# Kernel optimization log

Hardware: AMD Instinct MI355X
Metric: run time of the kernel (lower is better)

## Reference

```python
import jax, jax.numpy as jnp
import numpy as np

B, E, N1, K, CIN, CB, COUT, G = 2, 2048, 96, 32, 64, 32, 64, 4
NEG_SLOPE = 0.01  # nn.LeakyReLU default


def setup_inputs() -> dict:
    key = jax.random.key(0)
    ks = jax.random.split(key, 9)
    sites1 = jax.random.normal(ks[0], (B, N1, CIN), jnp.float32)
    sites2 = jax.random.normal(ks[1], (B, K, CIN), jnp.float32)
    bonds = jax.random.normal(ks[2], (B, E, CB), jnp.float32)
    idx1 = jax.random.randint(ks[3], (E,), 0, N1, jnp.int32)
    idx2 = jax.random.randint(ks[4], (E,), 0, K, jnp.int32)
    idx2_oh = jax.nn.one_hot(idx2, K, dtype=jnp.float32)  # [E, K]
    F = 2 * CIN + CB
    W_eq = jax.random.normal(ks[5], (G, F, COUT), jnp.float32) / np.float32(np.sqrt(F))
    b_eq = jnp.zeros((COUT,), jnp.float32)
    W_att = jax.random.normal(ks[6], (COUT, 1), jnp.float32) / np.float32(np.sqrt(COUT))
    b_att = jnp.zeros((1,), jnp.float32)
    # permutation group action on the K cells: identity + random perms
    perms = [jnp.arange(K, dtype=jnp.int32)]
    pk = ks[7]
    for _ in range(G - 1):
        pk, sk = jax.random.split(pk)
        perms.append(jax.random.permutation(sk, K).astype(jnp.int32))
    perms1 = jnp.stack(perms)  # [G, K]
    perms2 = perms1            # same action on input and output cell axes
    return dict(sites1=sites1, sites2=sites2, bonds=bonds, W_eq=W_eq, b_eq=b_eq,
                W_att=W_att, b_att=b_att, idx2_oh=idx2_oh, idx1=idx1, idx2=idx2,
                perms1=perms1, perms2=perms2)


def reference(sites1, sites2, bonds, W_eq, b_eq, W_att, b_att, idx2_oh, idx1, idx2, perms1, perms2):
    Bn = sites1.shape[0]
    Gn, Kn = perms1.shape
    On = W_eq.shape[2]
    # gather sender / receiver site features along the site axis
    sites_s = jnp.take(sites1, idx1, axis=1)              # [B,E,CIN]
    sites_r = jnp.take(sites2, idx2, axis=1)              # [B,E,CIN]
    vectors = jnp.concatenate([sites_s, sites_r, bonds], axis=2)  # [B,E,F]
    # outer-product expansion onto cells (idx2_oh is one-hot over K)
    vc = jnp.einsum('bef,ek->befk', vectors, idx2_oh)     # [B,E,F,K]
    # permutation-equivariant linear (group-averaged): per-group-element weight,
    # input cells permuted by perms1, output cells un-permuted by perms2
    xg = vc[:, :, :, perms1]                               # [B,E,F,G,K]
    yg = jnp.einsum('befgk,gfo->beogk', xg, W_eq)          # [B,E,O,G,K]
    inv2 = jnp.argsort(perms2, axis=1)                     # inverse perms [G,K]
    garr = jnp.arange(Gn)[:, None]
    y = yg[:, :, :, garr, inv2].mean(axis=3)               # [B,E,O,K]
    y = jax.nn.leaky_relu(y + b_eq[None, None, :, None], NEG_SLOPE)
    # gather each edge's receiving cell slot == dot with one-hot
    lat = jnp.einsum('beok,ek->beo', y, idx2_oh)           # [B,E,O]
    att = jax.nn.sigmoid(jnp.einsum('beo,oj->bej', lat, W_att) + b_att)  # [B,E,1]
    lat = att * lat
    # scatter_add over edges into receiving sites
    out = jnp.zeros((Bn, Kn, On), lat.dtype).at[:, idx2].add(lat)  # [B,K,O]
    return out
```

## Files before the change

kernel.cpp:

```cpp
#include <hip/hip_runtime.h>
#include <math.h>

#define Bn   2
#define En   2048
#define N1n  96
#define Kn   32
#define CINn 64
#define CBn  32
#define On   64
#define Gn   4
#define Fn   160
#define NEG  0.01f
#define NW   8
#define NT   (NW * 64)

__global__ void __launch_bounds__(NT, 1)
fused_kernel(const float* __restrict__ sites1, const float* __restrict__ sites2,
             const float* __restrict__ bonds,  const float* __restrict__ W_eq,
             const float* __restrict__ b_eq,   const float* __restrict__ W_att,
             const float* __restrict__ b_att,  const int* __restrict__ idx1,
             const int* __restrict__ idx2,     const int* __restrict__ perms1,
             const int* __restrict__ perms2,   float* __restrict__ out) {
    __shared__ float Weff[Fn][On];
    __shared__ float vbuf[NW][Fn];
    __shared__ float red[NW][On];
    __shared__ float s2[CINn];
    __shared__ float wgs[Gn];
    __shared__ int   elist[En];
    __shared__ int   ecount;

    const int t  = threadIdx.x;
    const int bk = blockIdx.x;
    const int b  = bk >> 5;
    const int k2 = bk & (Kn - 1);

    if (t < Gn) {
        int g = t, j = 0;
        for (; j < Kn; ++j) if (perms2[g * Kn + j] == k2) break;
        wgs[g] = (j < Kn && perms1[g * Kn + j] == k2) ? 1.f : 0.f;
    }
    if (t == Gn) ecount = 0;
    __syncthreads();

    {
        const float w0 = wgs[0], w1 = wgs[1], w2 = wgs[2], w3 = wgs[3];
        const float4* W4 = (const float4*)W_eq;
        float4* Wd = (float4*)&Weff[0][0];
        const int n4 = Fn * On / 4;
        for (int i = t; i < n4; i += NT) {
            float4 a0 = W4[i], a1 = W4[n4 + i], a2 = W4[2 * n4 + i], a3 = W4[3 * n4 + i];
            float4 r;
            r.x = 0.25f * (w0 * a0.x + w1 * a1.x + w2 * a2.x + w3 * a3.x);
            r.y = 0.25f * (w0 * a0.y + w1 * a1.y + w2 * a2.y + w3 * a3.y);
            r.z = 0.25f * (w0 * a0.z + w1 * a1.z + w2 * a2.z + w3 * a3.z);
            r.w = 0.25f * (w0 * a0.w + w1 * a1.w + w2 * a2.w + w3 * a3.w);
            Wd[i] = r;
        }
    }

    for (int e = t; e < En; e += NT)
        if (idx2[e] == k2) { int p = atomicAdd(&ecount, 1); elist[p] = e; }

    if (t < CINn) s2[t] = sites2[(b * Kn + k2) * CINn + t];
    __syncthreads();

    const int w    = t >> 6;
    const int lane = t & 63;
    const int og   = lane & 15;
    const int fg   = lane >> 4;

    const float4 be4 = ((const float4*)b_eq)[og];
    const float4 wa  = ((const float4*)W_att)[og];
    const float  ba  = b_att[0];
    const int    ec  = ecount;

    float4 oacc = make_float4(0.f, 0.f, 0.f, 0.f);

    for (int i = w; i < ec; i += NW) {
        const int e  = elist[i];
        const int i1 = idx1[e];

        vbuf[w][lane]        = sites1[(b * N1n + i1) * CINn + lane];
        vbuf[w][CINn + lane] = s2[lane];
        if (lane < CBn) vbuf[w][2 * CINn + lane] = bonds[(b * En + e) * CBn + lane];
        __builtin_amdgcn_wave_barrier();

        float4 acc = make_float4(0.f, 0.f, 0.f, 0.f);
#pragma unroll
        for (int fi = 0; fi < Fn / 4; ++fi) {
            const int f = 4 * fi + fg;
            const float  vf = vbuf[w][f];
            const float4 wv = *(const float4*)&Weff[f][og * 4];
            acc.x += vf * wv.x; acc.y += vf * wv.y;
            acc.z += vf * wv.z; acc.w += vf * wv.w;
        }
        __builtin_amdgcn_wave_barrier();

#pragma unroll
        for (int m = 16; m <= 32; m <<= 1) {
            acc.x += __shfl_xor(acc.x, m);
            acc.y += __shfl_xor(acc.y, m);
            acc.z += __shfl_xor(acc.z, m);
            acc.w += __shfl_xor(acc.w, m);
        }

        float4 lat;
        lat.x = acc.x + be4.x; lat.x = lat.x > 0.f ? lat.x : NEG * lat.x;
        lat.y = acc.y + be4.y; lat.y = lat.y > 0.f ? lat.y : NEG * lat.y;
        lat.z = acc.z + be4.z; lat.z = lat.z > 0.f ? lat.z : NEG * lat.z;
        lat.w = acc.w + be4.w; lat.w = lat.w > 0.f ? lat.w : NEG * lat.w;

        float part = lat.x * wa.x + lat.y * wa.y + lat.z * wa.z + lat.w * wa.w;
#pragma unroll
        for (int m = 1; m <= 8; m <<= 1) part += __shfl_xor(part, m);

        const float att = 1.f / (1.f + expf(-(part + ba)));
        oacc.x += att * lat.x;
        oacc.y += att * lat.y;
        oacc.z += att * lat.z;
        oacc.w += att * lat.w;
    }

    if (fg == 0) *(float4*)&red[w][og * 4] = oacc;
    __syncthreads();

    if (t < On) {
        float s = 0.f;
#pragma unroll
        for (int q = 0; q < NW; ++q) s += red[q][t];
        out[((size_t)b * Kn + k2) * On + t] = s;
    }
}

extern "C" void kernel_launch(void* const* d_in, const int* in_sizes, int n_in,
                              void* d_out, int out_size, void* d_ws, size_t ws_size,
                              hipStream_t stream) {
    const float* sites1 = (const float*)d_in[0];
    const float* sites2 = (const float*)d_in[1];
    const float* bonds  = (const float*)d_in[2];
    const float* W_eq   = (const float*)d_in[3];
    const float* b_eq   = (const float*)d_in[4];
    const float* W_att  = (const float*)d_in[5];
    const float* b_att  = (const float*)d_in[6];
    const int*   idx1   = (const int*)d_in[8];
    const int*   idx2   = (const int*)d_in[9];
    const int*   perms1 = (const int*)d_in[10];
    const int*   perms2 = (const int*)d_in[11];
    float* out = (float*)d_out;

    fused_kernel<<<Bn * Kn, NT, 0, stream>>>(
        sites1, sites2, bonds, W_eq, b_eq, W_att, b_att,
        idx1, idx2, perms1, perms2, out);
}
```

Measured before the change: 100.0 us.

## Batch eight edges per wave and hoist the constant receiver-site contribution

Each wave now loads eight edges' sender-site and bond features into shared memory at once. It then reuses every Weff float4 load across those eight accumulators, where before it ran one serial edge per iteration. The receiver-site part of the matvec is the same for every edge in a block, so it is computed once into p2 and used to seed the accumulators. This cuts redundant LDS traffic and serial loop latency and adds instruction-level parallelism. In exchange it uses more registers, and partial batches do duplicated padded work that is masked out.

```diff
diff --git a/kernel.cpp b/kernel.cpp
--- a/kernel.cpp
+++ b/kernel.cpp
@@ -13,6 +13,7 @@
 #define NEG  0.01f
 #define NW   8
 #define NT   (NW * 64)
+#define EB   8
 
 __global__ void __launch_bounds__(NT, 1)
 fused_kernel(const float* __restrict__ sites1, const float* __restrict__ sites2,
@@ -22,7 +23,7 @@
              const int* __restrict__ idx2,     const int* __restrict__ perms1,
              const int* __restrict__ perms2,   float* __restrict__ out) {
     __shared__ float Weff[Fn][On];
-    __shared__ float vbuf[NW][Fn];
+    __shared__ float vs[NW][EB][96];
     __shared__ float red[NW][On];
     __shared__ float s2[CINn];
     __shared__ float wgs[Gn];
@@ -68,57 +69,83 @@
     const int lane = t & 63;
     const int og   = lane & 15;
     const int fg   = lane >> 4;
+    const int ec   = ecount;
 
     const float4 be4 = ((const float4*)b_eq)[og];
     const float4 wa  = ((const float4*)W_att)[og];
     const float  ba  = b_att[0];
-    const int    ec  = ecount;
+
+    float4 p2 = make_float4(0.f, 0.f, 0.f, 0.f);
+#pragma unroll
+    for (int fi = 0; fi < 16; ++fi) {
+        const int f  = 64 + 4 * fi + fg;
+        const float  vf = s2[4 * fi + fg];
+        const float4 wv = *(const float4*)&Weff[f][og * 4];
+        p2.x += vf * wv.x; p2.y += vf * wv.y;
+        p2.z += vf * wv.z; p2.w += vf * wv.w;
+    }
 
     float4 oacc = make_float4(0.f, 0.f, 0.f, 0.f);
 
-    for (int i = w; i < ec; i += NW) {
-        const int e  = elist[i];
-        const int i1 = idx1[e];
+    for (int base = w * EB; base < ec; base += NW * EB) {
+        const int nb = (ec - base < EB) ? (ec - base) : EB;
 
-        vbuf[w][lane]        = sites1[(b * N1n + i1) * CINn + lane];
-        vbuf[w][CINn + lane] = s2[lane];
-        if (lane < CBn) vbuf[w][2 * CINn + lane] = bonds[(b * En + e) * CBn + lane];
+        __builtin_amdgcn_wave_barrier();
+#pragma unroll
+        for (int j = 0; j < EB; ++j) {
+            const int jj = j < nb ? j : nb - 1;
+            const int e  = elist[base + jj];
+            const int i1 = idx1[e];
+            vs[w][j][lane] = sites1[((b * N1n + i1) << 6) + lane];
+            if (lane < CBn) vs[w][j][CINn + lane] = bonds[(b * En + e) * CBn + lane];
+        }
         __builtin_amdgcn_wave_barrier();
 
-        float4 acc = make_float4(0.f, 0.f, 0.f, 0.f);
+        float4 acc[EB];
 #pragma unroll
-        for (int fi = 0; fi < Fn / 4; ++fi) {
-            const int f = 4 * fi + fg;
-            const float  vf = vbuf[w][f];
+        for (int j = 0; j < EB; ++j) acc[j] = p2;
+
+#pragma unroll
+        for (int fi = 0; fi < 24; ++fi) {
+            const int vsidx = 4 * fi + fg;
+            const int f     = vsidx < CINn ? vsidx : vsidx + CINn;
             const float4 wv = *(const float4*)&Weff[f][og * 4];
-            acc.x += vf * wv.x; acc.y += vf * wv.y;
-            acc.z += vf * wv.z; acc.w += vf * wv.w;
+#pragma unroll
+            for (int j = 0; j < EB; ++j) {
+                const float vf = vs[w][j][vsidx];
+                acc[j].x += vf * wv.x; acc[j].y += vf * wv.y;
+                acc[j].z += vf * wv.z; acc[j].w += vf * wv.w;
+            }
         }
         __builtin_amdgcn_wave_barrier();
 
 #pragma unroll
-        for (int m = 16; m <= 32; m <<= 1) {
-            acc.x += __shfl_xor(acc.x, m);
-            acc.y += __shfl_xor(acc.y, m);
-            acc.z += __shfl_xor(acc.z, m);
-            acc.w += __shfl_xor(acc.w, m);
+        for (int j = 0; j < EB; ++j) {
+            float4 a = acc[j];
+#pragma unroll
+            for (int m = 16; m <= 32; m <<= 1) {
+                a.x += __shfl_xor(a.x, m);
+                a.y += __shfl_xor(a.y, m);
+                a.z += __shfl_xor(a.z, m);
+                a.w += __shfl_xor(a.w, m);
+            }
+            float4 lat;
+            lat.x = a.x + be4.x; lat.x = lat.x > 0.f ? lat.x : NEG * lat.x;
+            lat.y = a.y + be4.y; lat.y = lat.y > 0.f ? lat.y : NEG * lat.y;
+            lat.z = a.z + be4.z; lat.z = lat.z > 0.f ? lat.z : NEG * lat.z;
+            lat.w = a.w + be4.w; lat.w = lat.w > 0.f ? lat.w : NEG * lat.w;
+
+            float part = lat.x * wa.x + lat.y * wa.y + lat.z * wa.z + lat.w * wa.w;
+#pragma unroll
+            for (int m = 1; m <= 8; m <<= 1) part += __shfl_xor(part, m);
+
+            float att = 1.f / (1.f + expf(-(part + ba)));
+            att *= (j < nb) ? 1.f : 0.f;
+            oacc.x += att * lat.x;
+            oacc.y += att * lat.y;
+            oacc.z += att * lat.z;
+            oacc.w += att * lat.w;
         }
-
-        float4 lat;
-        lat.x = acc.x + be4.x; lat.x = lat.x > 0.f ? lat.x : NEG * lat.x;
-        lat.y = acc.y + be4.y; lat.y = lat.y > 0.f ? lat.y : NEG * lat.y;
-        lat.z = acc.z + be4.z; lat.z = lat.z > 0.f ? lat.z : NEG * lat.z;
-        lat.w = acc.w + be4.w; lat.w = lat.w > 0.f ? lat.w : NEG * lat.w;
-
-        float part = lat.x * wa.x + lat.y * wa.y + lat.z * wa.z + lat.w * wa.w;
-#pragma unroll
-        for (int m = 1; m <= 8; m <<= 1) part += __shfl_xor(part, m);
-
-        const float att = 1.f / (1.f + expf(-(part + ba)));
-        oacc.x += att * lat.x;
-        oacc.y += att * lat.y;
-        oacc.z += att * lat.z;
-        oacc.w += att * lat.w;
     }
 
     if (fg == 0) *(float4*)&red[w][og * 4] = oacc;
```

Result: no change. 99.08 us (-0.9%).
